# Kernel optimization log

Measured on AMD Instinct MI355X. Metric: run time of the kernel, lower is better.

## Reference

```python
import jax, jax.numpy as jnp
import numpy as np

NUM_HEADS = 8
D_HEAD = 64
ATTENTION_WINDOW = 512


def alibi_bias(num_heads, q_len, k_len):
    # ALiBi slopes for power-of-2 number of heads (Press et al. 2021).
    start = 2.0 ** (-(2.0 ** -(np.log2(num_heads) - 3.0)))
    slopes = jnp.asarray([start * (start ** i) for i in range(num_heads)],
                         dtype=jnp.float32)  # [H]
    rel = jnp.arange(q_len)[:, None] - jnp.arange(k_len)[None, :]  # [t, T]
    # Bidirectional ALiBi: bias = -slope * |i - j|
    return -slopes[:, None, None] * jnp.abs(rel).astype(jnp.float32)  # [H, t, T]


def sliding_window_mask(seq_len, window):
    # Attend to tokens within window//2 on each side; even window -> window+1.
    if window % 2 == 0:
        window += 1
    half = window // 2
    idx = jnp.arange(seq_len)
    return jnp.abs(idx[:, None] - idx[None, :]) <= half  # [S, S] bool


def setup_inputs() -> dict:
    key = jax.random.key(0)
    ks = jax.random.split(key, 6)
    B, S, E = 2, 4096, 512
    HD = NUM_HEADS * D_HEAD
    s_in = 1.0 / np.sqrt(E)
    s_out = 1.0 / np.sqrt(HD)
    return {
        'inputs_q': jax.random.normal(ks[0], (B, S, E), jnp.float32),
        'inputs_kv': jax.random.normal(ks[1], (B, S, E), jnp.float32),
        'w_q': jax.random.normal(ks[2], (E, HD), jnp.float32) * s_in,
        'w_k': jax.random.normal(ks[3], (E, HD), jnp.float32) * s_in,
        'w_v': jax.random.normal(ks[4], (E, HD), jnp.float32) * s_in,
        'w_o': jax.random.normal(ks[5], (HD, E), jnp.float32) * s_out,
    }


def reference(inputs_q, inputs_kv, w_q, w_k, w_v, w_o):
    B, S, E = inputs_q.shape
    H, D = NUM_HEADS, D_HEAD
    q = (inputs_q @ w_q).reshape(B, S, H, D)
    k = (inputs_kv @ w_k).reshape(B, S, H, D)
    v = (inputs_kv @ w_v).reshape(B, S, H, D)
    # scores: [B, H, t, T]
    att = jnp.einsum('bthd,bThd->bhtT', q, k) * (1.0 / jnp.sqrt(jnp.float32(D)))
    att = att + alibi_bias(H, S, S)[None]
    mask = sliding_window_mask(S, ATTENTION_WINDOW)
    att = jnp.where(mask[None, None], att, jnp.finfo(jnp.float32).min)
    p = jax.nn.softmax(att, axis=-1)
    out = jnp.einsum('bhtT,bThd->bthd', p, v).reshape(B, S, H * D)
    return out @ w_o
```

## Files before the change

kernel.cpp:

```cpp
#include <hip/hip_runtime.h>

#define S_LEN  4096
#define NH     8
#define DH     64
#define EMB    512
#define HDIM   512
#define HALF_W 256
#define BATCH  2
#define M_ROWS (BATCH * S_LEN)

typedef __attribute__((ext_vector_type(8))) short bf16x8;
typedef __attribute__((ext_vector_type(4))) float f32x4;

__device__ __forceinline__ float b2f(unsigned short u) {
    union { unsigned int i; float f; } v; v.i = ((unsigned int)u) << 16; return v.f;
}
__device__ __forceinline__ unsigned short f2b(float f) {
    unsigned int x = __float_as_uint(f);
    unsigned int r = (x + 0x7fffu + ((x >> 16) & 1u)) >> 16;
    return (unsigned short)r;
}
__device__ __forceinline__ void unpack2(unsigned int u, float* d) {
    d[0] = b2f((unsigned short)(u & 0xffffu));
    d[1] = b2f((unsigned short)(u >> 16));
}
union FragU { uint4 u; bf16x8 f; };
__device__ __forceinline__ bf16x8 ldfrag(const unsigned short* p) {
    FragU x; x.u = *(const uint4*)p; return x.f;
}

__global__ void detect_dtype(const unsigned short* __restrict__ x, int* __restrict__ flag) {
    __shared__ int s;
    if (threadIdx.x == 0) s = 0;
    __syncthreads();
    int bad = 0;
    for (int i = threadIdx.x; i < 2048; i += 256) {
        float v = b2f(x[i]);
        if (!(fabsf(v) < 1.0e6f)) bad = 1;
    }
    if (bad) atomicOr(&s, 1);
    __syncthreads();
    if (threadIdx.x == 0) *flag = s;
}

__global__ __launch_bounds__(256) void transpose_w(
    const void* __restrict__ w0, const void* __restrict__ w1,
    const void* __restrict__ w2, const void* __restrict__ w3,
    unsigned short* __restrict__ out, const int* __restrict__ flag)
{
    __shared__ float t[32][33];
    const int z = blockIdx.z;
    const void* src = (z == 0) ? w0 : (z == 1) ? w1 : (z == 2) ? w2 : w3;
    unsigned short* dst = out + (size_t)z * EMB * EMB;
    const int k0 = blockIdx.y * 32, n0 = blockIdx.x * 32;
    const int kk = threadIdx.x >> 3;
    const int n4 = (threadIdx.x & 7) << 2;
    if (*flag) {
        float4 v = *(const float4*)((const float*)src + (size_t)(k0 + kk) * EMB + n0 + n4);
        t[kk][n4] = v.x; t[kk][n4 + 1] = v.y; t[kk][n4 + 2] = v.z; t[kk][n4 + 3] = v.w;
    } else {
        uint2 u = *(const uint2*)((const unsigned short*)src + (size_t)(k0 + kk) * EMB + n0 + n4);
        unpack2(u.x, &t[kk][n4]); unpack2(u.y, &t[kk][n4 + 2]);
    }
    __syncthreads();
    const int nn = threadIdx.x >> 3;
    const int ks = (threadIdx.x & 7) << 2;
    uint2 pk;
    pk.x = (unsigned int)f2b(t[ks + 0][nn]) | ((unsigned int)f2b(t[ks + 1][nn]) << 16);
    pk.y = (unsigned int)f2b(t[ks + 2][nn]) | ((unsigned int)f2b(t[ks + 3][nn]) << 16);
    *(uint2*)(dst + (size_t)(n0 + nn) * EMB + k0 + ks) = pk;
}

__global__ __launch_bounds__(256) void convert_in(
    const void* __restrict__ xq, const void* __restrict__ xkv,
    unsigned short* __restrict__ Xc, const int* __restrict__ flag)
{
    if (!*flag) return;
    const int z = blockIdx.y;
    const float* src = (const float*)(z ? xkv : xq);
    unsigned short* dst = Xc + (size_t)z * M_ROWS * EMB;
    const size_t base = ((size_t)blockIdx.x * 256 + threadIdx.x) * 8;
    float4 a = *(const float4*)(src + base);
    float4 b = *(const float4*)(src + base + 4);
    uint4 pk;
    pk.x = (unsigned int)f2b(a.x) | ((unsigned int)f2b(a.y) << 16);
    pk.y = (unsigned int)f2b(a.z) | ((unsigned int)f2b(a.w) << 16);
    pk.z = (unsigned int)f2b(b.x) | ((unsigned int)f2b(b.y) << 16);
    pk.w = (unsigned int)f2b(b.z) | ((unsigned int)f2b(b.w) << 16);
    *(uint4*)(dst + base) = pk;
}

#define GPAD 40

__device__ __forceinline__ void mgemm_core(
    const unsigned short* __restrict__ A, const unsigned short* __restrict__ Bt,
    int m0, f32x4 (*acc)[4],
    unsigned short (*A_lds)[GPAD], unsigned short (*B_lds)[GPAD])
{
    const int tid  = threadIdx.x;
    const int lane = tid & 63;
    const int w    = tid >> 6;
    const int wm   = (w >> 1) << 6;
    const int wn   = (w & 1) << 6;
    const int qcol = lane & 15;
    const int quad = lane >> 4;
    const int srow = tid >> 1;
    const int skh  = (tid & 1) << 4;

    for (int k0 = 0; k0 < EMB; k0 += 32) {
        const uint4* as = (const uint4*)(A + (size_t)(m0 + srow) * EMB + k0 + skh);
        uint4 ta0 = as[0], ta1 = as[1];
        const uint4* bs = (const uint4*)(Bt + (size_t)srow * EMB + k0 + skh);
        uint4 tb0 = bs[0], tb1 = bs[1];

        __syncthreads();
        *(uint4*)&A_lds[srow][skh]     = ta0;
        *(uint4*)&A_lds[srow][skh + 8] = ta1;
        *(uint4*)&B_lds[srow][skh]     = tb0;
        *(uint4*)&B_lds[srow][skh + 8] = tb1;
        __syncthreads();

        bf16x8 af[4], bf[4];
#pragma unroll
        for (int i = 0; i < 4; ++i) af[i] = ldfrag(&A_lds[wm + (i << 4) + qcol][quad * 8]);
#pragma unroll
        for (int j = 0; j < 4; ++j) bf[j] = ldfrag(&B_lds[wn + (j << 4) + qcol][quad * 8]);
#pragma unroll
        for (int i = 0; i < 4; ++i)
#pragma unroll
            for (int j = 0; j < 4; ++j)
                acc[i][j] = __builtin_amdgcn_mfma_f32_16x16x32_bf16(af[i], bf[j], acc[i][j], 0, 0, 0);
    }
}

__global__ __launch_bounds__(256) void gemm_qkv(
    const void* __restrict__ xq, const void* __restrict__ xkv,
    const unsigned short* __restrict__ Xc, const unsigned short* __restrict__ Wt,
    unsigned short* __restrict__ Qb, unsigned short* __restrict__ Kb,
    unsigned short* __restrict__ Vtb, const int* __restrict__ flag)
{
    __shared__ unsigned short A_lds[128][GPAD];
    __shared__ unsigned short B_lds[128][GPAD];
    const int n0 = blockIdx.x * 128;
    const int m0 = blockIdx.y * 128;
    const unsigned short* A;
    if (*flag) A = Xc + (n0 < 512 ? (size_t)0 : (size_t)M_ROWS * EMB);
    else       A = (const unsigned short*)(n0 < 512 ? xq : xkv);
    const unsigned short* Bt = Wt + (size_t)n0 * EMB;

    f32x4 acc[4][4];
#pragma unroll
    for (int i = 0; i < 4; ++i)
#pragma unroll
        for (int j = 0; j < 4; ++j) acc[i][j] = (f32x4){0.f, 0.f, 0.f, 0.f};

    mgemm_core(A, Bt, m0, acc, A_lds, B_lds);

    const int lane = threadIdx.x & 63, w = threadIdx.x >> 6;
    const int wm = (w >> 1) << 6, wn = (w & 1) << 6;
    const int qcol = lane & 15, quad = lane >> 4;
    const int mode = (n0 < 512) ? 0 : (n0 < 1024) ? 1 : 2;
#pragma unroll
    for (int ms = 0; ms < 4; ++ms)
#pragma unroll
        for (int ns = 0; ns < 4; ++ns)
#pragma unroll
            for (int r = 0; r < 4; ++r) {
                const int m = m0 + wm + (ms << 4) + (quad << 2) + r;
                const int n = n0 + wn + (ns << 4) + qcol;
                const unsigned short us = f2b(acc[ms][ns][r]);
                if (mode == 0) {
                    Qb[(size_t)m * HDIM + n] = us;
                } else if (mode == 1) {
                    Kb[(size_t)m * HDIM + (n - 512)] = us;
                } else {
                    const int hd = n - 1024;
                    const int bb = m >> 12, s = m & (S_LEN - 1);
                    const int hh = hd >> 6, d = hd & 63;
                    Vtb[((size_t)((bb * NH + hh) * DH + d)) * S_LEN + s] = us;
                }
            }
}

__global__ __launch_bounds__(256) void gemm_out(
    const unsigned short* __restrict__ A, const unsigned short* __restrict__ Bt,
    void* __restrict__ C, const int* __restrict__ flag)
{
    __shared__ unsigned short A_lds[128][GPAD];
    __shared__ unsigned short B_lds[128][GPAD];
    const int n0 = blockIdx.x * 128;
    const int m0 = blockIdx.y * 128;

    f32x4 acc[4][4];
#pragma unroll
    for (int i = 0; i < 4; ++i)
#pragma unroll
        for (int j = 0; j < 4; ++j) acc[i][j] = (f32x4){0.f, 0.f, 0.f, 0.f};

    mgemm_core(A, Bt + (size_t)n0 * EMB, m0, acc, A_lds, B_lds);

    const int lane = threadIdx.x & 63, w = threadIdx.x >> 6;
    const int wm = (w >> 1) << 6, wn = (w & 1) << 6;
    const int qcol = lane & 15, quad = lane >> 4;
    const int fp = *flag;
#pragma unroll
    for (int ms = 0; ms < 4; ++ms)
#pragma unroll
        for (int ns = 0; ns < 4; ++ns)
#pragma unroll
            for (int r = 0; r < 4; ++r) {
                const int m = m0 + wm + (ms << 4) + (quad << 2) + r;
                const int n = n0 + wn + (ns << 4) + qcol;
                const float v = acc[ms][ns][r];
                if (fp) ((float*)C)[(size_t)m * HDIM + n] = v;
                else    ((unsigned short*)C)[(size_t)m * HDIM + n] = f2b(v);
            }
}

__global__ __launch_bounds__(256) void attn_mfma(
    const unsigned short* __restrict__ Q,
    const unsigned short* __restrict__ Kg,
    const unsigned short* __restrict__ Vt,
    unsigned short* __restrict__ O)
{
    __shared__ __align__(16) unsigned short K_lds[64][72];
    __shared__ __align__(16) unsigned short V_lds[64][72];
    __shared__ __align__(16) unsigned short P_lds[4][16][72];

    const int tid  = threadIdx.x;
    const int lane = tid & 63;
    const int w    = tid >> 6;
    const int blk  = blockIdx.x;
    const int bh   = blk >> 6;
    const int r6   = blk & 63;
    const int tile = ((r6 & 7) << 3) | (r6 >> 3);
    const int h    = bh & (NH - 1);
    const int b    = bh >> 3;
    const int t0   = tile << 6;
    const int tq0  = t0 + (w << 4);

    const int qcol = lane & 15;
    const int quad = lane >> 4;
    const float slope = 1.0f / (float)(2 << h);

    const unsigned short* qrow = Q + (size_t)(b * S_LEN + tq0 + qcol) * HDIM + h * DH;
    const bf16x8 qf0 = ldfrag(qrow + quad * 8);
    const bf16x8 qf1 = ldfrag(qrow + 32 + quad * 8);

    f32x4 Oacc[4];
#pragma unroll
    for (int i = 0; i < 4; ++i) Oacc[i] = (f32x4){0.f, 0.f, 0.f, 0.f};
    float lsum = 0.f;

    for (int c = 0; c < 9; ++c) {
        const int j0 = t0 - HALF_W + (c << 6);
        __syncthreads();
#pragma unroll
        for (int p = 0; p < 2; ++p) {
            const int r  = (p << 5) + (tid >> 3);
            const int sg = (tid & 7) << 3;
            const int jc = min(max(j0 + r, 0), S_LEN - 1);
            *(uint4*)&K_lds[r][sg] =
                *(const uint4*)(Kg + (size_t)(b * S_LEN + jc) * HDIM + h * DH + sg);
            const int js = min(max(j0 + sg, 0), S_LEN - 8);
            *(uint4*)&V_lds[r][sg] =
                *(const uint4*)(Vt + ((size_t)((b * NH + h) * DH + r)) * S_LEN + js);
        }
        __syncthreads();

#pragma unroll
        for (int ks = 0; ks < 4; ++ks) {
            const bf16x8 kf0 = ldfrag(&K_lds[(ks << 4) + qcol][quad * 8]);
            const bf16x8 kf1 = ldfrag(&K_lds[(ks << 4) + qcol][32 + quad * 8]);
            f32x4 z = (f32x4){0.f, 0.f, 0.f, 0.f};
            z = __builtin_amdgcn_mfma_f32_16x16x32_bf16(kf0, qf0, z, 0, 0, 0);
            z = __builtin_amdgcn_mfma_f32_16x16x32_bf16(kf1, qf1, z, 0, 0, 0);
            unsigned short pb[4];
#pragma unroll
            for (int r = 0; r < 4; ++r) {
                const int j  = j0 + (ks << 4) + (quad << 2) + r;
                const int dd = (tq0 + qcol) - j;
                const bool ok = (j >= 0) && (j < S_LEN) && (dd <= HALF_W) && (dd >= -HALF_W);
                const float s = z[r] * 0.125f - slope * fabsf((float)dd);
                const float p = ok ? __expf(s - 12.0f) : 0.0f;
                lsum += p;
                pb[r] = f2b(p);
            }
            uint2 pk;
            pk.x = (unsigned int)pb[0] | ((unsigned int)pb[1] << 16);
            pk.y = (unsigned int)pb[2] | ((unsigned int)pb[3] << 16);
            *(uint2*)&P_lds[w][qcol][(ks << 4) + (quad << 2)] = pk;
        }

        const bf16x8 pf0 = ldfrag(&P_lds[w][qcol][quad * 8]);
        const bf16x8 pf1 = ldfrag(&P_lds[w][qcol][32 + quad * 8]);
#pragma unroll
        for (int ds = 0; ds < 4; ++ds) {
            const bf16x8 vf0 = ldfrag(&V_lds[(ds << 4) + qcol][quad * 8]);
            const bf16x8 vf1 = ldfrag(&V_lds[(ds << 4) + qcol][32 + quad * 8]);
            Oacc[ds] = __builtin_amdgcn_mfma_f32_16x16x32_bf16(vf0, pf0, Oacc[ds], 0, 0, 0);
            Oacc[ds] = __builtin_amdgcn_mfma_f32_16x16x32_bf16(vf1, pf1, Oacc[ds], 0, 0, 0);
        }
    }

    lsum += __shfl_xor(lsum, 16, 64);
    lsum += __shfl_xor(lsum, 32, 64);
    const float rz = 1.0f / lsum;

    unsigned short* obase = O + (size_t)(b * S_LEN + tq0 + qcol) * HDIM + h * DH;
#pragma unroll
    for (int ds = 0; ds < 4; ++ds) {
        uint2 pk;
        pk.x = (unsigned int)f2b(Oacc[ds][0] * rz) | ((unsigned int)f2b(Oacc[ds][1] * rz) << 16);
        pk.y = (unsigned int)f2b(Oacc[ds][2] * rz) | ((unsigned int)f2b(Oacc[ds][3] * rz) << 16);
        *(uint2*)(obase + (ds << 4) + (quad << 2)) = pk;
    }
}

extern "C" void kernel_launch(void* const* d_in, const int* in_sizes, int n_in,
                              void* d_out, int out_size, void* d_ws, size_t ws_size,
                              hipStream_t stream) {
    const void* xq  = d_in[0];
    const void* xkv = d_in[1];
    const void* wq  = d_in[2];
    const void* wk  = d_in[3];
    const void* wv  = d_in[4];
    const void* wo  = d_in[5];

    int* flag = (int*)d_ws;
    unsigned short* Qb  = (unsigned short*)((char*)d_ws + 256);
    unsigned short* Kb  = Qb  + (size_t)M_ROWS * HDIM;
    unsigned short* Vtb = Kb  + (size_t)M_ROWS * HDIM;
    unsigned short* Wt  = Vtb + (size_t)M_ROWS * HDIM;
    unsigned short* Wto = Wt + (size_t)3 * EMB * EMB;
    unsigned short* Xc  = (unsigned short*)d_out;

    detect_dtype<<<1, 256, 0, stream>>>((const unsigned short*)xq, flag);
    transpose_w<<<dim3(16, 16, 4), 256, 0, stream>>>(wq, wk, wv, wo, Wt, flag);
    convert_in<<<dim3(2048, 2), 256, 0, stream>>>(xq, xkv, Xc, flag);

    gemm_qkv<<<dim3(12, 64), 256, 0, stream>>>(xq, xkv, Xc, Wt, Qb, Kb, Vtb, flag);
    attn_mfma<<<BATCH * NH * (S_LEN / 64), 256, 0, stream>>>(Qb, Kb, Vtb, Qb);
    gemm_out<<<dim3(4, 64), 256, 0, stream>>>(Qb, Wto, d_out, flag);
}
```

Measured before the change: 190.8 us.

## Double the GEMM K-tile, prefetch next tile into registers, remap blocks per XCD

The shared GEMM core now stages a K=64 slice per iteration with wider LDS padding. It prefetches the next slice's global loads into registers while the current slice's MFMAs run, which halves the number of barriers and hides global latency. Both GEMM launches become 1D grids with an XCD-aware mapping, so blocks on the same XCD share M rows and get better L2 reuse. The cost is more LDS and registers per block, which may lower occupancy.

```diff
diff --git a/kernel.cpp b/kernel.cpp
--- a/kernel.cpp
+++ b/kernel.cpp
@@ -90,12 +90,12 @@
     *(uint4*)(dst + base) = pk;
 }
 
-#define GPAD 40
-
-__device__ __forceinline__ void mgemm_core(
+#define GP2 72
+
+__device__ __forceinline__ void mgemm_core2(
     const unsigned short* __restrict__ A, const unsigned short* __restrict__ Bt,
     int m0, f32x4 (*acc)[4],
-    unsigned short (*A_lds)[GPAD], unsigned short (*B_lds)[GPAD])
+    unsigned short (*A_lds)[GP2], unsigned short (*B_lds)[GP2])
 {
     const int tid  = threadIdx.x;
     const int lane = tid & 63;
@@ -105,31 +105,48 @@
     const int qcol = lane & 15;
     const int quad = lane >> 4;
     const int srow = tid >> 1;
-    const int skh  = (tid & 1) << 4;
-
-    for (int k0 = 0; k0 < EMB; k0 += 32) {
-        const uint4* as = (const uint4*)(A + (size_t)(m0 + srow) * EMB + k0 + skh);
-        uint4 ta0 = as[0], ta1 = as[1];
-        const uint4* bs = (const uint4*)(Bt + (size_t)srow * EMB + k0 + skh);
-        uint4 tb0 = bs[0], tb1 = bs[1];
-
+    const int sk   = (tid & 1) << 5;
+
+    const unsigned short* ap = A  + (size_t)(m0 + srow) * EMB + sk;
+    const unsigned short* bp = Bt + (size_t)srow * EMB + sk;
+
+    uint4 ra[4], rb[4];
+#pragma unroll
+    for (int i = 0; i < 4; ++i) {
+        ra[i] = *(const uint4*)(ap + i * 8);
+        rb[i] = *(const uint4*)(bp + i * 8);
+    }
+
+    for (int k0 = 0; k0 < EMB; k0 += 64) {
         __syncthreads();
-        *(uint4*)&A_lds[srow][skh]     = ta0;
-        *(uint4*)&A_lds[srow][skh + 8] = ta1;
-        *(uint4*)&B_lds[srow][skh]     = tb0;
-        *(uint4*)&B_lds[srow][skh + 8] = tb1;
+#pragma unroll
+        for (int i = 0; i < 4; ++i) {
+            *(uint4*)&A_lds[srow][sk + i * 8] = ra[i];
+            *(uint4*)&B_lds[srow][sk + i * 8] = rb[i];
+        }
         __syncthreads();
-
-        bf16x8 af[4], bf[4];
-#pragma unroll
-        for (int i = 0; i < 4; ++i) af[i] = ldfrag(&A_lds[wm + (i << 4) + qcol][quad * 8]);
-#pragma unroll
-        for (int j = 0; j < 4; ++j) bf[j] = ldfrag(&B_lds[wn + (j << 4) + qcol][quad * 8]);
-#pragma unroll
-        for (int i = 0; i < 4; ++i)
+        if (k0 + 64 < EMB) {
+#pragma unroll
+            for (int i = 0; i < 4; ++i) {
+                ra[i] = *(const uint4*)(ap + k0 + 64 + i * 8);
+                rb[i] = *(const uint4*)(bp + k0 + 64 + i * 8);
+            }
+        }
+#pragma unroll
+        for (int kh = 0; kh < 2; ++kh) {
+            bf16x8 af[4], bf[4];
+#pragma unroll
+            for (int i = 0; i < 4; ++i)
+                af[i] = ldfrag(&A_lds[wm + (i << 4) + qcol][(kh << 5) + quad * 8]);
 #pragma unroll
             for (int j = 0; j < 4; ++j)
-                acc[i][j] = __builtin_amdgcn_mfma_f32_16x16x32_bf16(af[i], bf[j], acc[i][j], 0, 0, 0);
+                bf[j] = ldfrag(&B_lds[wn + (j << 4) + qcol][(kh << 5) + quad * 8]);
+#pragma unroll
+            for (int i = 0; i < 4; ++i)
+#pragma unroll
+                for (int j = 0; j < 4; ++j)
+                    acc[i][j] = __builtin_amdgcn_mfma_f32_16x16x32_bf16(af[i], bf[j], acc[i][j], 0, 0, 0);
+        }
     }
 }
 
@@ -139,10 +156,14 @@
     unsigned short* __restrict__ Qb, unsigned short* __restrict__ Kb,
     unsigned short* __restrict__ Vtb, const int* __restrict__ flag)
 {
-    __shared__ unsigned short A_lds[128][GPAD];
-    __shared__ unsigned short B_lds[128][GPAD];
-    const int n0 = blockIdx.x * 128;
-    const int m0 = blockIdx.y * 128;
+    __shared__ unsigned short A_lds[128][GP2];
+    __shared__ unsigned short B_lds[128][GP2];
+    const int blk = blockIdx.x;
+    const int xcd = blk & 7, idx = blk >> 3;
+    const int mi = idx / 12, ni = idx - mi * 12;
+    const int m0 = ((xcd << 3) + mi) << 7;
+    const int n0 = ni << 7;
+
     const unsigned short* A;
     if (*flag) A = Xc + (n0 < 512 ? (size_t)0 : (size_t)M_ROWS * EMB);
     else       A = (const unsigned short*)(n0 < 512 ? xq : xkv);
@@ -154,7 +175,7 @@
 #pragma unroll
         for (int j = 0; j < 4; ++j) acc[i][j] = (f32x4){0.f, 0.f, 0.f, 0.f};
 
-    mgemm_core(A, Bt, m0, acc, A_lds, B_lds);
+    mgemm_core2(A, Bt, m0, acc, A_lds, B_lds);
 
     const int lane = threadIdx.x & 63, w = threadIdx.x >> 6;
     const int wm = (w >> 1) << 6, wn = (w & 1) << 6;
@@ -186,10 +207,13 @@
     const unsigned short* __restrict__ A, const unsigned short* __restrict__ Bt,
     void* __restrict__ C, const int* __restrict__ flag)
 {
-    __shared__ unsigned short A_lds[128][GPAD];
-    __shared__ unsigned short B_lds[128][GPAD];
-    const int n0 = blockIdx.x * 128;
-    const int m0 = blockIdx.y * 128;
+    __shared__ unsigned short A_lds[128][GP2];
+    __shared__ unsigned short B_lds[128][GP2];
+    const int blk = blockIdx.x;
+    const int xcd = blk & 7, idx = blk >> 3;
+    const int mi = idx >> 2, ni = idx & 3;
+    const int m0 = ((xcd << 3) + mi) << 7;
+    const int n0 = ni << 7;
 
     f32x4 acc[4][4];
 #pragma unroll
@@ -197,7 +221,7 @@
 #pragma unroll
         for (int j = 0; j < 4; ++j) acc[i][j] = (f32x4){0.f, 0.f, 0.f, 0.f};
 
-    mgemm_core(A, Bt + (size_t)n0 * EMB, m0, acc, A_lds, B_lds);
+    mgemm_core2(A, Bt + (size_t)n0 * EMB, m0, acc, A_lds, B_lds);
 
     const int lane = threadIdx.x & 63, w = threadIdx.x >> 6;
     const int wm = (w >> 1) << 6, wn = (w & 1) << 6;
@@ -339,7 +363,7 @@
     transpose_w<<<dim3(16, 16, 4), 256, 0, stream>>>(wq, wk, wv, wo, Wt, flag);
     convert_in<<<dim3(2048, 2), 256, 0, stream>>>(xq, xkv, Xc, flag);
 
-    gemm_qkv<<<dim3(12, 64), 256, 0, stream>>>(xq, xkv, Xc, Wt, Qb, Kb, Vtb, flag);
+    gemm_qkv<<<768, 256, 0, stream>>>(xq, xkv, Xc, Wt, Qb, Kb, Vtb, flag);
     attn_mfma<<<BATCH * NH * (S_LEN / 64), 256, 0, stream>>>(Qb, Kb, Vtb, Qb);
-    gemm_out<<<dim3(4, 64), 256, 0, stream>>>(Qb, Wto, d_out, flag);
-}
+    gemm_out<<<256, 256, 0, stream>>>(Qb, Wto, d_out, flag);
+}
```

Result: slower. 254.6 us (+33.4%).

## Use direct global-to-LDS loads in GEMMs and remap blocks per XCD

Applied to the files above, without the earlier changes.

Replaces the register-staged global-to-LDS copies in the projection GEMMs with global_load_lds direct transfers into unpadded 32-wide LDS tiles. It also flattens the grid and remaps block indices so blocks sharing an XCD work on nearby M rows, aiming for better L2 reuse. Removing the padding may add LDS bank conflicts on fragment reads. The loop keeps its single buffer with barriers, so load latency is still exposed.

```diff
diff --git a/kernel.cpp b/kernel.cpp
--- a/kernel.cpp
+++ b/kernel.cpp
@@ -27,6 +27,12 @@
 union FragU { uint4 u; bf16x8 f; };
 __device__ __forceinline__ bf16x8 ldfrag(const unsigned short* p) {
     FragU x; x.u = *(const uint4*)p; return x.f;
+}
+
+__device__ __forceinline__ void async16(const unsigned short* g, unsigned short* l) {
+    __builtin_amdgcn_global_load_lds(
+        (__attribute__((address_space(1))) void*)const_cast<unsigned short*>(g),
+        (__attribute__((address_space(3))) void*)l, 16, 0, 0);
 }
 
 __global__ void detect_dtype(const unsigned short* __restrict__ x, int* __restrict__ flag) {
@@ -90,12 +96,10 @@
     *(uint4*)(dst + base) = pk;
 }
 
-#define GPAD 40
-
-__device__ __forceinline__ void mgemm_core(
+__device__ __forceinline__ void mgemm_core3(
     const unsigned short* __restrict__ A, const unsigned short* __restrict__ Bt,
     int m0, f32x4 (*acc)[4],
-    unsigned short (*A_lds)[GPAD], unsigned short (*B_lds)[GPAD])
+    unsigned short (*A_lds)[32], unsigned short (*B_lds)[32])
 {
     const int tid  = threadIdx.x;
     const int lane = tid & 63;
@@ -104,20 +108,24 @@
     const int wn   = (w & 1) << 6;
     const int qcol = lane & 15;
     const int quad = lane >> 4;
-    const int srow = tid >> 1;
-    const int skh  = (tid & 1) << 4;
+
+    const int arow = (w << 4) + (lane >> 2);
+    const int acol = (lane & 3) << 3;
+
+    const unsigned short* gA = A  + (size_t)(m0 + arow) * EMB + acol;
+    const unsigned short* gB = Bt + (size_t)arow * EMB + acol;
+    unsigned short* lA0 = &A_lds[arow][acol];
+    unsigned short* lA1 = &A_lds[64 + arow][acol];
+    unsigned short* lB0 = &B_lds[arow][acol];
+    unsigned short* lB1 = &B_lds[64 + arow][acol];
+    const size_t half = (size_t)64 * EMB;
 
     for (int k0 = 0; k0 < EMB; k0 += 32) {
-        const uint4* as = (const uint4*)(A + (size_t)(m0 + srow) * EMB + k0 + skh);
-        uint4 ta0 = as[0], ta1 = as[1];
-        const uint4* bs = (const uint4*)(Bt + (size_t)srow * EMB + k0 + skh);
-        uint4 tb0 = bs[0], tb1 = bs[1];
-
         __syncthreads();
-        *(uint4*)&A_lds[srow][skh]     = ta0;
-        *(uint4*)&A_lds[srow][skh + 8] = ta1;
-        *(uint4*)&B_lds[srow][skh]     = tb0;
-        *(uint4*)&B_lds[srow][skh + 8] = tb1;
+        async16(gA + k0, lA0);
+        async16(gA + half + k0, lA1);
+        async16(gB + k0, lB0);
+        async16(gB + half + k0, lB1);
         __syncthreads();
 
         bf16x8 af[4], bf[4];
@@ -139,10 +147,14 @@
     unsigned short* __restrict__ Qb, unsigned short* __restrict__ Kb,
     unsigned short* __restrict__ Vtb, const int* __restrict__ flag)
 {
-    __shared__ unsigned short A_lds[128][GPAD];
-    __shared__ unsigned short B_lds[128][GPAD];
-    const int n0 = blockIdx.x * 128;
-    const int m0 = blockIdx.y * 128;
+    __shared__ __align__(16) unsigned short A_lds[128][32];
+    __shared__ __align__(16) unsigned short B_lds[128][32];
+    const int blk = blockIdx.x;
+    const int xcd = blk & 7, idx = blk >> 3;
+    const int mi = idx / 12, ni = idx - mi * 12;
+    const int m0 = ((xcd << 3) + mi) << 7;
+    const int n0 = ni << 7;
+
     const unsigned short* A;
     if (*flag) A = Xc + (n0 < 512 ? (size_t)0 : (size_t)M_ROWS * EMB);
     else       A = (const unsigned short*)(n0 < 512 ? xq : xkv);
@@ -154,7 +166,7 @@
 #pragma unroll
         for (int j = 0; j < 4; ++j) acc[i][j] = (f32x4){0.f, 0.f, 0.f, 0.f};
 
-    mgemm_core(A, Bt, m0, acc, A_lds, B_lds);
+    mgemm_core3(A, Bt, m0, acc, A_lds, B_lds);
 
     const int lane = threadIdx.x & 63, w = threadIdx.x >> 6;
     const int wm = (w >> 1) << 6, wn = (w & 1) << 6;
@@ -186,10 +198,13 @@
     const unsigned short* __restrict__ A, const unsigned short* __restrict__ Bt,
     void* __restrict__ C, const int* __restrict__ flag)
 {
-    __shared__ unsigned short A_lds[128][GPAD];
-    __shared__ unsigned short B_lds[128][GPAD];
-    const int n0 = blockIdx.x * 128;
-    const int m0 = blockIdx.y * 128;
+    __shared__ __align__(16) unsigned short A_lds[128][32];
+    __shared__ __align__(16) unsigned short B_lds[128][32];
+    const int blk = blockIdx.x;
+    const int xcd = blk & 7, idx = blk >> 3;
+    const int mi = idx >> 2, ni = idx & 3;
+    const int m0 = ((xcd << 3) + mi) << 7;
+    const int n0 = ni << 7;
 
     f32x4 acc[4][4];
 #pragma unroll
@@ -197,7 +212,7 @@
 #pragma unroll
         for (int j = 0; j < 4; ++j) acc[i][j] = (f32x4){0.f, 0.f, 0.f, 0.f};
 
-    mgemm_core(A, Bt + (size_t)n0 * EMB, m0, acc, A_lds, B_lds);
+    mgemm_core3(A, Bt + (size_t)n0 * EMB, m0, acc, A_lds, B_lds);
 
     const int lane = threadIdx.x & 63, w = threadIdx.x >> 6;
     const int wm = (w >> 1) << 6, wn = (w & 1) << 6;
@@ -339,7 +354,7 @@
     transpose_w<<<dim3(16, 16, 4), 256, 0, stream>>>(wq, wk, wv, wo, Wt, flag);
     convert_in<<<dim3(2048, 2), 256, 0, stream>>>(xq, xkv, Xc, flag);
 
-    gemm_qkv<<<dim3(12, 64), 256, 0, stream>>>(xq, xkv, Xc, Wt, Qb, Kb, Vtb, flag);
+    gemm_qkv<<<768, 256, 0, stream>>>(xq, xkv, Xc, Wt, Qb, Kb, Vtb, flag);
     attn_mfma<<<BATCH * NH * (S_LEN / 64), 256, 0, stream>>>(Qb, Kb, Vtb, Qb);
-    gemm_out<<<dim3(4, 64), 256, 0, stream>>>(Qb, Wto, d_out, flag);
-}
+    gemm_out<<<256, 256, 0, stream>>>(Qb, Wto, d_out, flag);
+}
```

Measured after the change: 183.3 us. 3.9% less time.
